# Optimization experiments

Hardware: AMD Instinct MI355X
Metric: run time of the kernel (lower is better)

The kernel has to match this reference:

```python
import jax, jax.numpy as jnp
import numpy as np

T, IN, OUT, MEM, M = 2048, 1024, 4096, 256, 8192
HG, HL = MEM // 2, 256  # GRU hidden per direction, LSTM hidden per direction


def _gru_dir(x, Wih, Whh, bih, bhh, reverse):
    # x: [T, D]; PyTorch GRU gate order: r, z, n
    H = Whh.shape[-1]
    xg = x @ Wih.T + bih  # [T, 3H], precompute input projections
    def step(h, g):
        gr, gz, gn = jnp.split(g, 3)
        hr, hz, hn = jnp.split(h @ Whh.T + bhh, 3)
        r = jax.nn.sigmoid(gr + hr)
        z = jax.nn.sigmoid(gz + hz)
        n = jnp.tanh(gn + r * hn)
        hnew = (1.0 - z) * n + z * h
        return hnew, hnew
    _, hs = jax.lax.scan(step, jnp.zeros((H,), x.dtype), xg, reverse=reverse)
    return hs  # [T, H]


def _bigru(x, Wih, Whh, bih, bhh):
    f = _gru_dir(x, Wih[0], Whh[0], bih[0], bhh[0], False)
    b = _gru_dir(x, Wih[1], Whh[1], bih[1], bhh[1], True)
    return jnp.concatenate([f, b], axis=-1)  # [T, 2H]


def _lstm_dir(x, Wih, Whh, bih, bhh, reverse):
    # PyTorch LSTM gate order: i, f, g, o
    H = Whh.shape[-1]
    xg = x @ Wih.T + bih  # [T, 4H]
    def step(carry, g):
        h, cst = carry
        gi, gf, gg, go = jnp.split(g + h @ Whh.T + bhh, 4)
        i = jax.nn.sigmoid(gi)
        f = jax.nn.sigmoid(gf)
        gg = jnp.tanh(gg)
        o = jax.nn.sigmoid(go)
        cst = f * cst + i * gg
        h = o * jnp.tanh(cst)
        return (h, cst), h
    z = jnp.zeros((H,), x.dtype)
    _, hs = jax.lax.scan(step, (z, z), xg, reverse=reverse)
    return hs


def _bilstm(x, Wih, Whh, bih, bhh):
    f = _lstm_dir(x, Wih[0], Whh[0], bih[0], bhh[0], False)
    b = _lstm_dir(x, Wih[1], Whh[1], bih[1], bhh[1], True)
    return jnp.concatenate([f, b], axis=-1)


def setup_inputs() -> dict:
    key = jax.random.key(0)
    ks = iter(jax.random.split(key, 32))
    r = lambda *s: jax.random.normal(next(ks), s, jnp.float32) * 0.05
    return {
        "c": jax.random.normal(next(ks), (T, IN), jnp.float32),
        "memory": jax.random.normal(next(ks), (M, MEM), jnp.float32),
        "enc_Wih": r(2, 3 * HG, IN), "enc_Whh": r(2, 3 * HG, HG),
        "enc_bih": r(2, 3 * HG), "enc_bhh": r(2, 3 * HG),
        "cenc_Wih": r(2, 3 * HG, IN), "cenc_Whh": r(2, 3 * HG, HG),
        "cenc_bih": r(2, 3 * HG), "cenc_bhh": r(2, 3 * HG),
        "know_W": r(IN, MEM), "know_b": r(IN),
        "lstm0_Wih": r(2, 4 * HL, IN), "lstm0_Whh": r(2, 4 * HL, HL),
        "lstm0_bih": r(2, 4 * HL), "lstm0_bhh": r(2, 4 * HL),
        "lstm1_Wih": r(2, 4 * HL, 2 * HL), "lstm1_Whh": r(2, 4 * HL, HL),
        "lstm1_bih": r(2, 4 * HL), "lstm1_bhh": r(2, 4 * HL),
        "out_W": r(OUT, 2 * HL), "out_b": r(OUT),
    }


def reference(c, memory, enc_Wih, enc_Whh, enc_bih, enc_bhh,
              cenc_Wih, cenc_Whh, cenc_bih, cenc_bhh, know_W, know_b,
              lstm0_Wih, lstm0_Whh, lstm0_bih, lstm0_bhh,
              lstm1_Wih, lstm1_Whh, lstm1_bih, lstm1_bhh, out_W, out_b):
    # contextual encoding, appended to memory in the original (detached state)
    c_memory = _bigru(c, cenc_Wih, cenc_Whh, cenc_bih, cenc_bhh)[-1]  # [256]
    # utterance encoding
    u = _bigru(c, enc_Wih, enc_Whh, enc_bih, enc_bhh)[-1]  # [256]
    # attention over memory bank: replaces the original per-item Python loop
    p = jax.nn.softmax(memory @ u)  # [M]
    h = p @ memory                   # [256]
    o = (u + h) @ know_W.T + know_b  # [IN]
    x = c + o                        # broadcast over T
    x = _bilstm(x, lstm0_Wih, lstm0_Whh, lstm0_bih, lstm0_bhh)  # [T, 512]
    x = _bilstm(x, lstm1_Wih, lstm1_Whh, lstm1_bih, lstm1_bhh)  # [T, 512]
    out = jax.nn.softmax(x @ out_W.T + out_b, axis=1)  # [T, OUT]
    return out, c_memory
```

## Files before the change

kernel.cpp:

```cpp
#include <hip/hip_runtime.h>
#include <hip/hip_bf16.h>

static constexpr int kT    = 2048;
static constexpr int kOUT_ELEMS = 2048 * 4096;

typedef _Float16 half2_t __attribute__((ext_vector_type(2)));
typedef _Float16 half8_t __attribute__((ext_vector_type(8)));
typedef float f32x4_t __attribute__((ext_vector_type(4)));
typedef unsigned long long u64;

__device__ __forceinline__ unsigned pack_h2(float a, float b) {
  half2_t h{(_Float16)a, (_Float16)b};
  return __builtin_bit_cast(unsigned, h);
}
__device__ __forceinline__ float fdot2u(unsigned a, unsigned b, float c) {
  return __builtin_amdgcn_fdot2(__builtin_bit_cast(half2_t, a),
                                __builtin_bit_cast(half2_t, b), c, false);
}
__device__ __forceinline__ float sigm(float x) {
  return 1.f / (1.f + __expf(-x));
}
__device__ __forceinline__ float tanh_f(float x) {
  float ax = fabsf(x);
  float e = __expf(-2.f * ax);
  float r = (1.f - e) / (1.f + e);
  return x < 0.f ? -r : r;
}

__global__ __launch_bounds__(256) void prep_kernel(
    const float* __restrict__ c_in,
    const float* __restrict__ enc_Wih, const float* __restrict__ enc_bih,
    const float* __restrict__ cenc_Wih, const float* __restrict__ cenc_bih,
    const float* __restrict__ enc_Whh, const float* __restrict__ cenc_Whh,
    const float* __restrict__ l0_Wih, const float* __restrict__ l0_Whh,
    const float* __restrict__ l1_Wih, const float* __restrict__ l1_Whh,
    const float* __restrict__ out_W,
    const float* __restrict__ l0_bih, const float* __restrict__ l0_bhh,
    const float* __restrict__ l1_bih, const float* __restrict__ l1_bhh,
    float* __restrict__ bcat,
    float* __restrict__ bias0, float* __restrict__ bias1,
    unsigned* __restrict__ wprep5, unsigned* __restrict__ wgru,
    u64* __restrict__ payz,
    _Float16* __restrict__ c16, _Float16* __restrict__ wcat16,
    _Float16* __restrict__ l0W16, _Float16* __restrict__ l1W16,
    _Float16* __restrict__ outW16) {
  int idx0 = blockIdx.x * blockDim.x + threadIdx.x;
  int stride = gridDim.x * blockDim.x;
  for (int i = idx0; i < 1024; i += stride) payz[i] = 0ull;
  for (int i = idx0; i < 768; i += stride)
    bcat[i] = (i < 384) ? enc_bih[i] : cenc_bih[i - 384];
  for (int i = idx0; i < 2048; i += stride) {
    bias0[i] = l0_bih[i] + l0_bhh[i];
    bias1[i] = l1_bih[i] + l1_bhh[i];
  }
  for (int i = idx0; i < 4 * 4 * 128 * 256; i += stride) {
    int j = i & 255;
    int e = (i >> 8) & 127;
    int p = (i >> 15) & 3;
    int ld = i >> 17;
    const float* W = (ld < 2 ? l0_Whh : l1_Whh) + (ld & 1) * 1024 * 256;
    int gate = j >> 6, m = j & 63;
    int R = gate * 256 + 64 * p + m;
    wprep5[i] = pack_h2(W[R * 256 + 2 * e], W[R * 256 + 2 * e + 1]);
  }
  for (int i = idx0; i < 2 * 64 * 384; i += stride) {
    int row = i % 384;
    int e = (i / 384) & 63;
    int g2 = i / (64 * 384);
    const float* W = g2 ? cenc_Whh : enc_Whh;
    wgru[i] = pack_h2(W[row * 128 + 2 * e], W[row * 128 + 2 * e + 1]);
  }
  for (int i = idx0; i < 2048 * 1024; i += stride) c16[i] = (_Float16)c_in[i];
  for (int i = idx0; i < 768 * 1024; i += stride) {
    int r = i >> 10, cc = i & 1023;
    float v = (r < 384) ? enc_Wih[r * 1024 + cc] : cenc_Wih[(r - 384) * 1024 + cc];
    wcat16[i] = (_Float16)v;
  }
  for (int i = idx0; i < 2048 * 1024; i += stride) l0W16[i] = (_Float16)l0_Wih[i];
  for (int i = idx0; i < 2048 * 512; i += stride)  l1W16[i] = (_Float16)l1_Wih[i];
  for (int i = idx0; i < 4096 * 512; i += stride)  outW16[i] = (_Float16)out_W[i];
}

__global__ __launch_bounds__(256) void cvt16(
    const float* __restrict__ in, _Float16* __restrict__ out, int n) {
  int i = (blockIdx.x * 256 + threadIdx.x) * 4;
  if (i < n) {
    float4 v = *(const float4*)&in[i];
    out[i + 0] = (_Float16)v.x;
    out[i + 1] = (_Float16)v.y;
    out[i + 2] = (_Float16)v.z;
    out[i + 3] = (_Float16)v.w;
  }
}

__global__ __launch_bounds__(256) void gemm_mfma(
    const _Float16* __restrict__ A,
    const _Float16* __restrict__ B,
    const float* __restrict__ bias,
    float* __restrict__ C,
    int M, int N, int K) {
  const int wave = threadIdx.x >> 6, lane = threadIdx.x & 63;
  const int r = lane & 15, kg = lane >> 4;
  const int m0 = blockIdx.y * 64 + wave * 16;
  const int n0 = blockIdx.x * 64;
  const _Float16* ap = A + (size_t)(m0 + r) * K + kg * 8;
  const _Float16* bp = B + (size_t)(n0 + r) * K + kg * 8;
  f32x4_t acc0 = {0.f, 0.f, 0.f, 0.f};
  f32x4_t acc1 = {0.f, 0.f, 0.f, 0.f};
  f32x4_t acc2 = {0.f, 0.f, 0.f, 0.f};
  f32x4_t acc3 = {0.f, 0.f, 0.f, 0.f};
  for (int k0 = 0; k0 < K; k0 += 32) {
    half8_t av = *(const half8_t*)(ap + k0);
    half8_t b0 = *(const half8_t*)(bp + k0);
    half8_t b1 = *(const half8_t*)(bp + (size_t)16 * K + k0);
    half8_t b2 = *(const half8_t*)(bp + (size_t)32 * K + k0);
    half8_t b3 = *(const half8_t*)(bp + (size_t)48 * K + k0);
    acc0 = __builtin_amdgcn_mfma_f32_16x16x32_f16(av, b0, acc0, 0, 0, 0);
    acc1 = __builtin_amdgcn_mfma_f32_16x16x32_f16(av, b1, acc1, 0, 0, 0);
    acc2 = __builtin_amdgcn_mfma_f32_16x16x32_f16(av, b2, acc2, 0, 0, 0);
    acc3 = __builtin_amdgcn_mfma_f32_16x16x32_f16(av, b3, acc3, 0, 0, 0);
  }
  float bv0 = bias ? bias[n0 + r]      : 0.f;
  float bv1 = bias ? bias[n0 + 16 + r] : 0.f;
  float bv2 = bias ? bias[n0 + 32 + r] : 0.f;
  float bv3 = bias ? bias[n0 + 48 + r] : 0.f;
  const int row0 = m0 + 4 * kg;
#pragma unroll
  for (int i = 0; i < 4; ++i) {
    float* cr = C + (size_t)(row0 + i) * N + n0 + r;
    cr[0]  = acc0[i] + bv0;
    cr[16] = acc1[i] + bv1;
    cr[32] = acc2[i] + bv2;
    cr[48] = acc3[i] + bv3;
  }
}

__global__ __launch_bounds__(256) void gru2(
    const float* __restrict__ xgg,
    const float* __restrict__ c_in,
    const unsigned* __restrict__ wgru,
    const float* __restrict__ enc_Wih, const float* __restrict__ enc_bih,
    const float* __restrict__ enc_bhh,
    const float* __restrict__ cenc_Wih, const float* __restrict__ cenc_bih,
    const float* __restrict__ cenc_bhh,
    float* __restrict__ u_out, float* __restrict__ cmem_out) {
  int b = blockIdx.x, j = threadIdx.x;
  __shared__ __align__(16) unsigned h2g[64];
  __shared__ float zs[128];
  const bool dual = j < 128;
  if (b < 2) {
    const unsigned* wg = wgru + b * (64 * 384);
    const float* bhh = b ? cenc_bhh : enc_bhh;
    unsigned w0[64], w1[64];
#pragma unroll
    for (int e = 0; e < 64; ++e) w0[e] = wg[e * 384 + j];
#pragma unroll
    for (int e = 0; e < 64; ++e) asm volatile("" : "+v"(w0[e]));
    float bh0 = bhh[j], bh1 = 0.f;
    if (dual) {
#pragma unroll
      for (int e = 0; e < 64; ++e) w1[e] = wg[e * 384 + 256 + j];
#pragma unroll
      for (int e = 0; e < 64; ++e) asm volatile("" : "+v"(w1[e]));
      bh1 = bhh[256 + j];
    }
    if (j < 64) h2g[j] = 0u;
    float hreg = 0.f;
    __syncthreads();
    const float* xp = xgg + b * 384;
    float x0 = xp[j];
    float x1 = dual ? xp[256 + j] : 0.f;
    for (int t = 0; t < kT; ++t) {
      float x0n = 0.f, x1n = 0.f;
      if (t + 1 < kT) {
        x0n = xp[(t + 1) * 768 + j];
        if (dual) x1n = xp[(t + 1) * 768 + 256 + j];
      }
      const uint4* h4 = (const uint4*)h2g;
      float a0 = 0.f, a1 = 0.f;
#pragma unroll
      for (int k = 0; k < 16; ++k) {
        uint4 hh = h4[k];
        a0 = fdot2u(w0[4 * k + 0], hh.x, a0);
        a0 = fdot2u(w0[4 * k + 1], hh.y, a0);
        a0 = fdot2u(w0[4 * k + 2], hh.z, a0);
        a0 = fdot2u(w0[4 * k + 3], hh.w, a0);
        if (dual) {
          a1 = fdot2u(w1[4 * k + 0], hh.x, a1);
          a1 = fdot2u(w1[4 * k + 1], hh.y, a1);
          a1 = fdot2u(w1[4 * k + 2], hh.z, a1);
          a1 = fdot2u(w1[4 * k + 3], hh.w, a1);
        }
      }
      if (!dual) zs[j - 128] = sigm(x0 + a0 + bh0);
      __syncthreads();
      if (dual) {
        float r = sigm(x0 + a0 + bh0);
        float n = tanh_f(x1 + r * (a1 + bh1));
        float z = zs[j];
        hreg = (1.f - z) * n + z * hreg;
        float hx = __shfl_xor(hreg, 1);
        if (!(j & 1)) h2g[j >> 1] = pack_h2(hreg, hx);
      }
      __syncthreads();
      x0 = x0n; x1 = x1n;
    }
    if (dual) { if (b == 0) u_out[j] = hreg; else cmem_out[j] = hreg; }
  } else {
    const float* Wih = ((b == 2) ? enc_Wih : cenc_Wih) + 384 * 1024;
    const float* bih = ((b == 2) ? enc_bih : cenc_bih) + 384;
    const float* bhh = ((b == 2) ? enc_bhh : cenc_bhh) + 384;
    const float* crow = c_in + (long)(kT - 1) * 1024;
    float a0 = bih[j], a1 = 0.f;
    {
      const float* wr = Wih + (long)j * 1024;
      for (int k = 0; k < 1024; k += 4) {
        float4 cv = *(const float4*)&crow[k];
        float4 wv = *(const float4*)&wr[k];
        a0 += cv.x * wv.x + cv.y * wv.y + cv.z * wv.z + cv.w * wv.w;
      }
    }
    if (dual) {
      a1 = bih[256 + j];
      const float* wr = Wih + (long)(256 + j) * 1024;
      for (int k = 0; k < 1024; k += 4) {
        float4 cv = *(const float4*)&crow[k];
        float4 wv = *(const float4*)&wr[k];
        a1 += cv.x * wv.x + cv.y * wv.y + cv.z * wv.z + cv.w * wv.w;
      }
    }
    if (!dual) zs[j - 128] = sigm(a0 + bhh[j]);
    __syncthreads();
    if (dual) {
      float r = sigm(a0 + bhh[j]);
      float n = tanh_f(a1 + r * bhh[256 + j]);
      float z = zs[j];
      float h = (1.f - z) * n;
      if (b == 2) u_out[128 + j] = h; else cmem_out[128 + j] = h;
    }
  }
}

__global__ __launch_bounds__(256) void attn_dots(
    const float* __restrict__ mem, const float* __restrict__ u, float* __restrict__ d) {
  __shared__ float us[256];
  int tid = threadIdx.x;
  us[tid] = u[tid];
  __syncthreads();
  int g = tid >> 3, l8 = tid & 7;
  int row = blockIdx.x * 32 + g;
  const float* mr = mem + (long)row * 256 + l8 * 32;
  float p = 0.f;
#pragma unroll
  for (int k = 0; k < 32; k += 4) {
    float4 m4 = *(const float4*)&mr[k];
    p += m4.x * us[l8 * 32 + k] + m4.y * us[l8 * 32 + k + 1] +
         m4.z * us[l8 * 32 + k + 2] + m4.w * us[l8 * 32 + k + 3];
  }
  p += __shfl_down(p, 4);
  p += __shfl_down(p, 2);
  p += __shfl_down(p, 1);
  if (l8 == 0) d[row] = p;
}

__global__ __launch_bounds__(1024) void attn_soft(
    const float* __restrict__ d, float* __restrict__ p, float* __restrict__ h_acc) {
  __shared__ float red[1024];
  int tid = threadIdx.x;
  float v[8];
  float mx = -1e30f;
#pragma unroll
  for (int i = 0; i < 8; i++) { v[i] = d[tid * 8 + i]; mx = fmaxf(mx, v[i]); }
  red[tid] = mx; __syncthreads();
  for (int s = 512; s > 0; s >>= 1) {
    if (tid < s) red[tid] = fmaxf(red[tid], red[tid + s]);
    __syncthreads();
  }
  mx = red[0]; __syncthreads();
  float sm = 0.f; float e[8];
#pragma unroll
  for (int i = 0; i < 8; i++) { e[i] = __expf(v[i] - mx); sm += e[i]; }
  red[tid] = sm; __syncthreads();
  for (int s = 512; s > 0; s >>= 1) {
    if (tid < s) red[tid] += red[tid + s];
    __syncthreads();
  }
  float rz = 1.f / red[0];
#pragma unroll
  for (int i = 0; i < 8; i++) p[tid * 8 + i] = e[i] * rz;
  if (tid < 256) h_acc[tid] = 0.f;
}

__global__ __launch_bounds__(256) void attn_h(
    const float* __restrict__ mem, const float* __restrict__ p, float* __restrict__ h_acc) {
  int tid = threadIdx.x;
  int r0 = blockIdx.x * 128;
  float acc = 0.f;
  for (int i = 0; i < 128; i++) acc += p[r0 + i] * mem[(long)(r0 + i) * 256 + tid];
  atomicAdd(&h_acc[tid], acc);
}

__global__ __launch_bounds__(128) void attn_o(
    const float* __restrict__ u, const float* __restrict__ h_acc,
    const float* __restrict__ know_W, const float* __restrict__ know_b,
    float* __restrict__ o) {
  __shared__ float uh[256];
  int tid = threadIdx.x;
  uh[tid] = u[tid] + h_acc[tid];
  uh[128 + tid] = u[128 + tid] + h_acc[128 + tid];
  __syncthreads();
  int row = blockIdx.x * 128 + tid;
  float acc = know_b[row];
  for (int k = 0; k < 256; k += 4) {
    float4 w4 = *(const float4*)&know_W[row * 256 + k];
    acc += w4.x * uh[k] + w4.y * uh[k + 1] + w4.z * uh[k + 2] + w4.w * uh[k + 3];
  }
  o[row] = acc;
}

__global__ __launch_bounds__(128) void attn_ov(
    const float* __restrict__ o, const float* __restrict__ Wih0, float* __restrict__ ov) {
  int row = blockIdx.x * 128 + threadIdx.x;
  float acc = 0.f;
  for (int k = 0; k < 1024; k += 4) {
    float4 w4 = *(const float4*)&Wih0[(long)row * 1024 + k];
    float4 o4 = *(const float4*)&o[k];
    acc += w4.x * o4.x + w4.y * o4.y + w4.z * o4.z + w4.w * o4.w;
  }
  ov[row] = acc;
}

__global__ __launch_bounds__(256) void lstm_cc4(
    const unsigned* __restrict__ wp5,
    const float* __restrict__ xg,
    const float* __restrict__ extra,
    float* __restrict__ out,
    u64* __restrict__ pay) {
  const int bid = blockIdx.x;
  const int xs = bid & 7;
  if (xs >= 2) return;
  const int dir = xs, p = bid >> 3;
  const int j = threadIdx.x;
  const int gate = j >> 6;
  const int m = j & 63;
  const int R = gate * 256 + 64 * p + m;

  __shared__ __align__(16) unsigned h2v[128];
  __shared__ float gact[256];

  const unsigned* base = wp5 + (size_t)dir * 131072 + (size_t)p * 32768;
  unsigned wv[128];
#pragma unroll
  for (int e = 0; e < 128; ++e) wv[e] = base[e * 256 + j];
#pragma unroll
  for (int e = 0; e < 128; ++e) asm volatile("" : "+v"(wv[e]));

  float exv = extra ? extra[dir * 1024 + R] : 0.f;
  if (j < 128) h2v[j] = 0u;
  float cst = 0.f;
  __syncthreads();

  const int bi = dir * 4 + p;
  u64* mypay = pay + bi * 64;
  const int pi = (j < 96) ? (j >> 5) : 0;
  const int pp = pi + (pi >= p ? 1 : 0);
  u64* peerpay = pay + (dir * 4 + pp) * 64;
  const int pidx = j & 31;

  const float* xp = xg + dir * 1024;
  const int t0 = dir ? (kT - 1) : 0;
  const int dt = dir ? -1 : 1;
  float xc = xp[(long)t0 * 2048 + R] + exv;

  for (int s = 0; s < kT; ++s) {
    const int t = t0 + s * dt;
    float xn_ = 0.f;
    if (s + 1 < kT) xn_ = xp[(long)(t + dt) * 2048 + R];
    if (j < 96 && s > 0) {
      u64 v;
      int guard = 0;
      do {
        v = __hip_atomic_load(&peerpay[(s & 1) * 32 + pidx],
                              __ATOMIC_RELAXED, __HIP_MEMORY_SCOPE_AGENT);
      } while ((unsigned)(v >> 32) < (unsigned)s && ++guard < (1 << 18));
      h2v[32 * pp + pidx] = (unsigned)v;
    }
    __syncthreads();
    const uint4* h4 = (const uint4*)h2v;
    float acc = xc;
#pragma unroll
    for (int c = 0; c < 32; ++c) {
      uint4 hh = h4[c];
      acc = fdot2u(wv[4 * c + 0], hh.x, acc);
      acc = fdot2u(wv[4 * c + 1], hh.y, acc);
      acc = fdot2u(wv[4 * c + 2], hh.z, acc);
      acc = fdot2u(wv[4 * c + 3], hh.w, acc);
    }
    float act = (gate == 2) ? tanh_f(acc) : sigm(acc);
    gact[j] = act;
    __syncthreads();
    if (j < 64) {
      float iv  = gact[j];
      float fv  = gact[64 + j];
      float gv  = gact[128 + j];
      float ovv = gact[192 + j];
      cst = fv * cst + iv * gv;
      float h = ovv * tanh_f(cst);
      out[(long)t * 512 + dir * 256 + 64 * p + j] = h;
      float hx = __shfl_xor(h, 1);
      if (!(j & 1)) {
        int idx = j >> 1;
        unsigned hp = pack_h2(h, hx);
        h2v[32 * p + idx] = hp;
        u64 tagged = ((u64)(unsigned)(s + 1) << 32) | (u64)hp;
        __hip_atomic_store(&mypay[((s + 1) & 1) * 32 + idx], tagged,
                           __ATOMIC_RELAXED, __HIP_MEMORY_SCOPE_AGENT);
      }
    }
    xc = xn_ + exv;
  }
}

__global__ __launch_bounds__(256) void softmax_rows(
    const float* __restrict__ logits, float* __restrict__ outp) {
  int t = blockIdx.x, tid = threadIdx.x;
  __shared__ float red[256];
  const float* lr = logits + (long)t * 4096;
  float v[16];
  float mx = -1e30f;
#pragma unroll
  for (int i = 0; i < 16; i++) { v[i] = lr[tid + 256 * i]; mx = fmaxf(mx, v[i]); }
  red[tid] = mx; __syncthreads();
  for (int s = 128; s > 0; s >>= 1) {
    if (tid < s) red[tid] = fmaxf(red[tid], red[tid + s]);
    __syncthreads();
  }
  mx = red[0]; __syncthreads();
  float sm = 0.f;
#pragma unroll
  for (int i = 0; i < 16; i++) { v[i] = __expf(v[i] - mx); sm += v[i]; }
  red[tid] = sm; __syncthreads();
  for (int s = 128; s > 0; s >>= 1) {
    if (tid < s) red[tid] += red[tid + s];
    __syncthreads();
  }
  float rz = 1.f / red[0];
#pragma unroll
  for (int i = 0; i < 16; i++) outp[(long)t * 4096 + tid + 256 * i] = v[i] * rz;
}

extern "C" void kernel_launch(void* const* d_in, const int* in_sizes, int n_in,
                              void* d_out, int out_size, void* d_ws, size_t ws_size,
                              hipStream_t stream) {
  const float* c        = (const float*)d_in[0];
  const float* memory   = (const float*)d_in[1];
  const float* enc_Wih  = (const float*)d_in[2];
  const float* enc_Whh  = (const float*)d_in[3];
  const float* enc_bih  = (const float*)d_in[4];
  const float* enc_bhh  = (const float*)d_in[5];
  const float* cenc_Wih = (const float*)d_in[6];
  const float* cenc_Whh = (const float*)d_in[7];
  const float* cenc_bih = (const float*)d_in[8];
  const float* cenc_bhh = (const float*)d_in[9];
  const float* know_W   = (const float*)d_in[10];
  const float* know_b   = (const float*)d_in[11];
  const float* l0_Wih   = (const float*)d_in[12];
  const float* l0_Whh   = (const float*)d_in[13];
  const float* l0_bih   = (const float*)d_in[14];
  const float* l0_bhh   = (const float*)d_in[15];
  const float* l1_Wih   = (const float*)d_in[16];
  const float* l1_Whh   = (const float*)d_in[17];
  const float* l1_bih   = (const float*)d_in[18];
  const float* l1_bhh   = (const float*)d_in[19];
  const float* out_W    = (const float*)d_in[20];
  const float* out_b    = (const float*)d_in[21];

  float* ws = (float*)d_ws;
  float* outp = (float*)d_out;

  float* xgg   = ws;
  float* cW    = ws + 1572864;
  float* l0out = ws + 6553600;
  float* xg1   = ws + 7602176;
  unsigned* wprep5 = (unsigned*)(ws + 11796480);
  float* bcat  = ws + 12320768;
  float* bias0 = ws + 12321536;
  float* bias1 = ws + 12323584;
  float* u_vec = ws + 12325632;
  float* d_att = ws + 12325888;
  float* p_att = ws + 12334080;
  float* h_acc = ws + 12342272;
  float* o_vec = ws + 12342528;
  float* ov    = ws + 12343552;
  float* l1out = ws + 12345600;
  unsigned* wgru = (unsigned*)(ws + 13656320);
  u64* payload = (u64*)(ws + 13705472);
  float* logits = ws;

  _Float16* c16     = (_Float16*)(ws + 12345600);
  _Float16* wcat16  = (_Float16*)(ws + 7602176);
  _Float16* l0W16   = (_Float16*)(ws + 7995392);
  _Float16* l0out16 = (_Float16*)(ws + 1572864);
  _Float16* l1out16 = (_Float16*)(ws + 9043968);
  _Float16* l1W16   = (_Float16*)(ws + 13707520);
  _Float16* outW16  = (_Float16*)(ws + 14231808);

  prep_kernel<<<512, 256, 0, stream>>>(c, enc_Wih, enc_bih, cenc_Wih, cenc_bih,
                                       enc_Whh, cenc_Whh,
                                       l0_Wih, l0_Whh, l1_Wih, l1_Whh, out_W,
                                       l0_bih, l0_bhh, l1_bih, l1_bhh,
                                       bcat, bias0, bias1, wprep5, wgru, payload,
                                       c16, wcat16, l0W16, l1W16, outW16);
  gemm_mfma<<<dim3(12, 32), 256, 0, stream>>>(c16, wcat16, bcat, xgg, 2048, 768, 1024);
  gemm_mfma<<<dim3(32, 32), 256, 0, stream>>>(c16, l0W16, bias0, cW, 2048, 2048, 1024);
  gru2<<<4, 256, 0, stream>>>(xgg, c, wgru, enc_Wih, enc_bih, enc_bhh,
                              cenc_Wih, cenc_bih, cenc_bhh,
                              u_vec, outp + kOUT_ELEMS);
  attn_dots<<<256, 256, 0, stream>>>(memory, u_vec, d_att);
  attn_soft<<<1, 1024, 0, stream>>>(d_att, p_att, h_acc);
  attn_h<<<64, 256, 0, stream>>>(memory, p_att, h_acc);
  attn_o<<<8, 128, 0, stream>>>(u_vec, h_acc, know_W, know_b, o_vec);
  attn_ov<<<16, 128, 0, stream>>>(o_vec, l0_Wih, ov);
  lstm_cc4<<<32, 256, 0, stream>>>(wprep5, cW, ov, l0out, payload);
  cvt16<<<1024, 256, 0, stream>>>(l0out, l0out16, 2048 * 512);
  gemm_mfma<<<dim3(32, 32), 256, 0, stream>>>(l0out16, l1W16, bias1, xg1, 2048, 2048, 512);
  lstm_cc4<<<32, 256, 0, stream>>>(wprep5 + 262144, xg1, nullptr, l1out, payload + 512);
  cvt16<<<1024, 256, 0, stream>>>(l1out, l1out16, 2048 * 512);
  gemm_mfma<<<dim3(64, 32), 256, 0, stream>>>(l1out16, outW16, out_b, logits, 2048, 4096, 512);
  softmax_rows<<<2048, 256, 0, stream>>>(logits, outp);
}
```

Baseline: 7.184 ms.

## Spread GRU gates over 384 threads and split recurrent weights between registers and LDS

The GRU recurrence kernel now launches 384 threads per block, one thread per gate row, instead of 256 threads where half of them computed two gate rows. Each thread keeps 40 of its 64 packed fp16 weight words in registers and reads the other 24 from shared memory. The aim is to shorten the serial per-timestep dot product and even out the load across threads on the critical recurrent path. In exchange, each step adds LDS weight reads and more threads taking part in the barriers.

```diff
diff --git a/kernel.cpp b/kernel.cpp
--- a/kernel.cpp
+++ b/kernel.cpp
@@ -135,7 +135,7 @@
   }
 }
 
-__global__ __launch_bounds__(256) void gru2(
+__global__ __launch_bounds__(384) void gru3(
     const float* __restrict__ xgg,
     const float* __restrict__ c_in,
     const unsigned* __restrict__ wgru,
@@ -144,99 +144,82 @@
     const float* __restrict__ cenc_Wih, const float* __restrict__ cenc_bih,
     const float* __restrict__ cenc_bhh,
     float* __restrict__ u_out, float* __restrict__ cmem_out) {
-  int b = blockIdx.x, j = threadIdx.x;
+  const int b = blockIdx.x, j = threadIdx.x;
+  const int gate = j >> 7, m = j & 127;
   __shared__ __align__(16) unsigned h2g[64];
-  __shared__ float zs[128];
-  const bool dual = j < 128;
+  __shared__ float rv[128], zv[128];
+  __shared__ __align__(16) unsigned wl[384 * 26];
   if (b < 2) {
     const unsigned* wg = wgru + b * (64 * 384);
     const float* bhh = b ? cenc_bhh : enc_bhh;
-    unsigned w0[64], w1[64];
-#pragma unroll
-    for (int e = 0; e < 64; ++e) w0[e] = wg[e * 384 + j];
-#pragma unroll
-    for (int e = 0; e < 64; ++e) asm volatile("" : "+v"(w0[e]));
-    float bh0 = bhh[j], bh1 = 0.f;
-    if (dual) {
-#pragma unroll
-      for (int e = 0; e < 64; ++e) w1[e] = wg[e * 384 + 256 + j];
-#pragma unroll
-      for (int e = 0; e < 64; ++e) asm volatile("" : "+v"(w1[e]));
-      bh1 = bhh[256 + j];
-    }
+    unsigned wv[40];
+#pragma unroll
+    for (int e = 0; e < 40; ++e) wv[e] = wg[e * 384 + j];
+#pragma unroll
+    for (int e2 = 0; e2 < 24; ++e2) wl[j * 26 + e2] = wg[(40 + e2) * 384 + j];
+    const float bh = bhh[j];
     if (j < 64) h2g[j] = 0u;
     float hreg = 0.f;
     __syncthreads();
-    const float* xp = xgg + b * 384;
-    float x0 = xp[j];
-    float x1 = dual ? xp[256 + j] : 0.f;
+    const float* xp = xgg + b * 384 + j;
+    float xc = xp[0];
     for (int t = 0; t < kT; ++t) {
-      float x0n = 0.f, x1n = 0.f;
-      if (t + 1 < kT) {
-        x0n = xp[(t + 1) * 768 + j];
-        if (dual) x1n = xp[(t + 1) * 768 + 256 + j];
+      float xn = 0.f;
+      if (t + 1 < kT) xn = xp[(t + 1) * 768];
+      const uint4* h4 = (const uint4*)h2g;
+      float a = 0.f;
+#pragma unroll
+      for (int k = 0; k < 10; ++k) {
+        uint4 hh = h4[k];
+        a = fdot2u(wv[4 * k + 0], hh.x, a);
+        a = fdot2u(wv[4 * k + 1], hh.y, a);
+        a = fdot2u(wv[4 * k + 2], hh.z, a);
+        a = fdot2u(wv[4 * k + 3], hh.w, a);
       }
-      const uint4* h4 = (const uint4*)h2g;
-      float a0 = 0.f, a1 = 0.f;
-#pragma unroll
-      for (int k = 0; k < 16; ++k) {
-        uint4 hh = h4[k];
-        a0 = fdot2u(w0[4 * k + 0], hh.x, a0);
-        a0 = fdot2u(w0[4 * k + 1], hh.y, a0);
-        a0 = fdot2u(w0[4 * k + 2], hh.z, a0);
-        a0 = fdot2u(w0[4 * k + 3], hh.w, a0);
-        if (dual) {
-          a1 = fdot2u(w1[4 * k + 0], hh.x, a1);
-          a1 = fdot2u(w1[4 * k + 1], hh.y, a1);
-          a1 = fdot2u(w1[4 * k + 2], hh.z, a1);
-          a1 = fdot2u(w1[4 * k + 3], hh.w, a1);
-        }
+#pragma unroll
+      for (int k = 0; k < 6; ++k) {
+        uint4 hh = h4[10 + k];
+        uint4 qw = *(const uint4*)&wl[j * 26 + 4 * k];
+        a = fdot2u(qw.x, hh.x, a);
+        a = fdot2u(qw.y, hh.y, a);
+        a = fdot2u(qw.z, hh.z, a);
+        a = fdot2u(qw.w, hh.w, a);
       }
-      if (!dual) zs[j - 128] = sigm(x0 + a0 + bh0);
+      if (gate == 0)      rv[m] = sigm(xc + a + bh);
+      else if (gate == 1) zv[m] = sigm(xc + a + bh);
       __syncthreads();
-      if (dual) {
-        float r = sigm(x0 + a0 + bh0);
-        float n = tanh_f(x1 + r * (a1 + bh1));
-        float z = zs[j];
+      if (gate == 2) {
+        float r = rv[m], z = zv[m];
+        float n = tanh_f(xc + r * (a + bh));
         hreg = (1.f - z) * n + z * hreg;
         float hx = __shfl_xor(hreg, 1);
-        if (!(j & 1)) h2g[j >> 1] = pack_h2(hreg, hx);
+        if (!(m & 1)) h2g[m >> 1] = pack_h2(hreg, hx);
       }
       __syncthreads();
-      x0 = x0n; x1 = x1n;
+      xc = xn;
     }
-    if (dual) { if (b == 0) u_out[j] = hreg; else cmem_out[j] = hreg; }
+    if (gate == 2) { if (b == 0) u_out[m] = hreg; else cmem_out[m] = hreg; }
   } else {
     const float* Wih = ((b == 2) ? enc_Wih : cenc_Wih) + 384 * 1024;
     const float* bih = ((b == 2) ? enc_bih : cenc_bih) + 384;
     const float* bhh = ((b == 2) ? enc_bhh : cenc_bhh) + 384;
     const float* crow = c_in + (long)(kT - 1) * 1024;
-    float a0 = bih[j], a1 = 0.f;
-    {
-      const float* wr = Wih + (long)j * 1024;
-      for (int k = 0; k < 1024; k += 4) {
-        float4 cv = *(const float4*)&crow[k];
-        float4 wv = *(const float4*)&wr[k];
-        a0 += cv.x * wv.x + cv.y * wv.y + cv.z * wv.z + cv.w * wv.w;
-      }
+    float a = bih[j];
+    const float* wr = Wih + (long)j * 1024;
+    for (int k = 0; k < 1024; k += 4) {
+      float4 cv = *(const float4*)&crow[k];
+      float4 wv4 = *(const float4*)&wr[k];
+      a += cv.x * wv4.x + cv.y * wv4.y + cv.z * wv4.z + cv.w * wv4.w;
     }
-    if (dual) {
-      a1 = bih[256 + j];
-      const float* wr = Wih + (long)(256 + j) * 1024;
-      for (int k = 0; k < 1024; k += 4) {
-        float4 cv = *(const float4*)&crow[k];
-        float4 wv = *(const float4*)&wr[k];
-        a1 += cv.x * wv.x + cv.y * wv.y + cv.z * wv.z + cv.w * wv.w;
-      }
-    }
-    if (!dual) zs[j - 128] = sigm(a0 + bhh[j]);
-    __syncthreads();
-    if (dual) {
-      float r = sigm(a0 + bhh[j]);
-      float n = tanh_f(a1 + r * bhh[256 + j]);
-      float z = zs[j];
+    const float bh = bhh[j];
+    if (gate == 0)      rv[m] = sigm(a + bh);
+    else if (gate == 1) zv[m] = sigm(a + bh);
+    __syncthreads();
+    if (gate == 2) {
+      float r = rv[m], z = zv[m];
+      float n = tanh_f(a + r * bh);
       float h = (1.f - z) * n;
-      if (b == 2) u_out[128 + j] = h; else cmem_out[128 + j] = h;
+      if (b == 2) u_out[128 + m] = h; else cmem_out[128 + m] = h;
     }
   }
 }
@@ -513,7 +496,7 @@
                                        c16, wcat16, l0W16, l1W16, outW16);
   gemm_mfma<<<dim3(12, 32), 256, 0, stream>>>(c16, wcat16, bcat, xgg, 2048, 768, 1024);
   gemm_mfma<<<dim3(32, 32), 256, 0, stream>>>(c16, l0W16, bias0, cW, 2048, 2048, 1024);
-  gru2<<<4, 256, 0, stream>>>(xgg, c, wgru, enc_Wih, enc_bih, enc_bhh,
+  gru3<<<4, 384, 0, stream>>>(xgg, c, wgru, enc_Wih, enc_bih, enc_bhh,
                               cenc_Wih, cenc_bih, cenc_bhh,
                               u_vec, outp + kOUT_ELEMS);
   attn_dots<<<256, 256, 0, stream>>>(memory, u_vec, d_att);
```

Result: slower. 7.371 ms (+2.6%).
